# Kernel tuning notes

Measured on AMD Instinct MI355X. Metric: run time of the kernel, lower is better.

Reference implementation:

```python
import jax, jax.numpy as jnp
import numpy as np

N_HEAD = 16
QK_NOPE = 128
QK_ROPE = 64
QK_HEAD = QK_NOPE + QK_ROPE  # 192
V_HEAD = 128
SCALE = 1.0 / np.sqrt(QK_HEAD)


def setup_inputs() -> dict:
    key = jax.random.key(0)
    ks = jax.random.split(key, 8)
    B, T, C = 2, 2048, 2048
    s = lambda fan: 1.0 / np.sqrt(fan)
    return {
        "x": jax.random.normal(ks[0], (B, T, C), jnp.float32),
        "freqs_cis": jax.random.uniform(ks[1], (T, QK_ROPE // 2, 2), jnp.float32),
        "w_q": jax.random.normal(ks[2], (C, N_HEAD * QK_HEAD), jnp.float32) * s(C),
        "w_kv_down": jax.random.normal(ks[3], (C, 256), jnp.float32) * s(C),
        "w_k_up": jax.random.normal(ks[4], (256, N_HEAD * QK_HEAD), jnp.float32) * s(256),
        "w_v_up": jax.random.normal(ks[5], (256, N_HEAD * V_HEAD), jnp.float32) * s(256),
        "w_o": jax.random.normal(ks[6], (N_HEAD * V_HEAD, C), jnp.float32) * s(N_HEAD * V_HEAD),
        "start_pos": 0,
    }


def _rotate_half(x):
    x1, x2 = x[..., : x.shape[-1] // 2], x[..., x.shape[-1] // 2 :]
    return jnp.concatenate([-x2, x1], axis=-1)


def reference(x, freqs_cis, w_q, w_kv_down, w_k_up, w_v_up, w_o, start_pos):
    B, T, C = x.shape
    # low-rank MLA projections
    q = (x @ w_q).reshape(B, T, N_HEAD, QK_HEAD)
    kv = x @ w_kv_down                                  # (B,T,r)
    k = (kv @ w_k_up).reshape(B, T, N_HEAD, QK_HEAD)
    v = (kv @ w_v_up).reshape(B, T, N_HEAD, V_HEAD)

    # inline RoPE on decoupled rope dims
    q_nope, q_rope = q[..., :QK_NOPE], q[..., QK_NOPE:]
    k_nope, k_rope = k[..., :QK_NOPE], k[..., QK_NOPE:]
    freqs = freqs_cis[start_pos : start_pos + T]         # (T, 32, 2)
    cos = freqs[..., 0][None, :, None, :]                # (1,T,1,32)
    sin = freqs[..., 1][None, :, None, :]
    rep = QK_ROPE // cos.shape[-1]
    cos = jnp.tile(cos, (1, 1, 1, rep))                  # (1,T,1,64)
    sin = jnp.tile(sin, (1, 1, 1, rep))
    q_rope = q_rope * cos + _rotate_half(q_rope) * sin
    k_rope = k_rope * cos + _rotate_half(k_rope) * sin
    q = jnp.concatenate([q_nope, q_rope], axis=-1)
    k = jnp.concatenate([k_nope, k_rope], axis=-1)

    # causal SDPA with mismatched QK vs V head dims
    scores = jnp.einsum("bqhd,bkhd->bhqk", q, k) * SCALE
    causal = jnp.tril(jnp.ones((T, T), dtype=bool))
    scores = jnp.where(causal[None, None], scores, -jnp.inf)
    probs = jax.nn.softmax(scores, axis=-1)
    out = jnp.einsum("bhqk,bkhd->bqhd", probs, v)        # (B,T,H,V_HEAD)
    out = out.reshape(B, T, N_HEAD * V_HEAD)
    return out @ w_o
```

## Files before the change

kernel.cpp:

```cpp
#include <hip/hip_runtime.h>
#include <stdint.h>

typedef unsigned short u16;
typedef float f32x4 __attribute__((ext_vector_type(4)));
typedef __bf16 bf16x8 __attribute__((ext_vector_type(8)));

static __device__ __forceinline__ u16 f2bf(float f) {
  union { float f; unsigned u; } v; v.f = f;
  unsigned r = v.u + 0x7fffu + ((v.u >> 16) & 1u);
  return (u16)(r >> 16);
}
static __device__ __forceinline__ float bf2f(u16 h) {
  union { unsigned u; float f; } v; v.u = ((unsigned)h) << 16;
  return v.f;
}

#define GLD_LDS16(gp, lp) __builtin_amdgcn_global_load_lds( \
    (__attribute__((address_space(1))) void*)(gp),          \
    (__attribute__((address_space(3))) void*)(lp), 16, 0, 0)

#define MFMA16(a, b, c) __builtin_amdgcn_mfma_f32_16x16x32_bf16((a), (b), (c), 0, 0, 0)

__global__ void prep_kernel(const float* __restrict__ x, u16* __restrict__ xb,
                            const float* __restrict__ w_q, u16* __restrict__ wqT,
                            const float* __restrict__ w_kvd, u16* __restrict__ wkdT,
                            const float* __restrict__ w_ku, u16* __restrict__ wkuT,
                            const float* __restrict__ w_vu, u16* __restrict__ wvuT,
                            const float* __restrict__ w_o, u16* __restrict__ woT) {
  __shared__ float tile[32][33];
  const int bid = blockIdx.x;
  const int tx = threadIdx.x, ty = threadIdx.y;
  if (bid < 2048) {
    const int tid = ty * 32 + tx;
    const long n = 4096ll * 2048;
    const long stride = 2048ll * 256 * 4;
    for (long i = ((long)bid * 256 + tid) * 4; i < n; i += stride) {
      float4 v = *(const float4*)(x + i);
      union { u16 s[4]; uint2 u; } pk;
      pk.s[0] = f2bf(v.x); pk.s[1] = f2bf(v.y); pk.s[2] = f2bf(v.z); pk.s[3] = f2bf(v.w);
      *(uint2*)(xb + i) = pk.u;
    }
    return;
  }
  const float* W; u16* WT; int K, N, bx, by;
  int r = bid - 2048;
  if (r < 6144)        { W = w_q;   WT = wqT;  K = 2048; N = 3072; bx = r % 96; by = r / 96; }
  else if ((r -= 6144) < 512) { W = w_kvd; WT = wkdT; K = 2048; N = 256;  bx = r % 8;  by = r / 8; }
  else if ((r -= 512) < 768)  { W = w_ku;  WT = wkuT; K = 256;  N = 3072; bx = r % 96; by = r / 96; }
  else if ((r -= 768) < 512)  { W = w_vu;  WT = wvuT; K = 256;  N = 2048; bx = r % 64; by = r / 64; }
  else                 { r -= 512; W = w_o; WT = woT; K = 2048; N = 2048; bx = r % 64; by = r / 64; }
  const int n0 = bx * 32, k0 = by * 32;
#pragma unroll
  for (int i = 0; i < 32; i += 8) tile[ty + i][tx] = W[(long)(k0 + ty + i) * N + n0 + tx];
  __syncthreads();
#pragma unroll
  for (int i = 0; i < 32; i += 8)
    WT[(long)(n0 + ty + i) * K + k0 + tx] = f2bf(tile[tx][ty + i]);
}

__device__ __forceinline__ void epilogue_rope_store(
    u16* __restrict__ C, const int N, const f32x4 (*acc)[4],
    const int m0, const int wr, const int wc, const int cbase_wave,
    const int lrow, const int lg, const bool ropewin,
    const float* __restrict__ freqs, const int sp) {
#pragma unroll
  for (int mi = 0; mi < 4; mi++) {
    const int r0 = m0 + (wr << 6) + (mi << 4) + (lg << 2);
#pragma unroll
    for (int r = 0; r < 4; r++) {
      float v0 = acc[mi][0][r], v1 = acc[mi][1][r];
      float v2 = acc[mi][2][r], v3 = acc[mi][3][r];
      if (ropewin) {
        const int t = (r0 + r) & 2047;
        const float2 cs0 = *(const float2*)&freqs[((long)(sp + t) * 32 + lrow) * 2];
        const float2 cs1 = *(const float2*)&freqs[((long)(sp + t) * 32 + 16 + lrow) * 2];
        const float n0v = v0 * cs0.x - v2 * cs0.y;
        const float n1v = v1 * cs1.x - v3 * cs1.y;
        const float n2v = v2 * cs0.x + v0 * cs0.y;
        const float n3v = v3 * cs1.x + v1 * cs1.y;
        v0 = n0v; v1 = n1v; v2 = n2v; v3 = n3v;
      }
      const long ro = (long)(r0 + r) * N + cbase_wave + lrow;
      C[ro] = f2bf(v0);
      C[ro + 16] = f2bf(v1);
      C[ro + 32] = f2bf(v2);
      C[ro + 48] = f2bf(v3);
    }
  }
}

__global__ __launch_bounds__(256, 2)
void gemm_q_kvd_kernel(const u16* __restrict__ A, const u16* __restrict__ wqT,
                       const u16* __restrict__ wkdT, u16* __restrict__ qb,
                       u16* __restrict__ kvb,
                       const float* __restrict__ freqs, const int* __restrict__ sp_ptr) {
  constexpr int K = 2048;
  const int bid = blockIdx.x;
  const int xcd = bid & 7;
  const int idx = bid >> 3;
  const int m0 = ((xcd << 2) + (idx & 3)) << 7;
  const int n0raw = (idx >> 2) << 7;
  const bool is_kv = n0raw >= 3072;
  const u16* BT = is_kv ? (wkdT + (long)(n0raw - 3072) * K) : (wqT + (long)n0raw * K);
  u16* C = is_kv ? kvb : qb;
  const int N = is_kv ? 256 : 3072;
  const int c_base = is_kv ? (n0raw - 3072) : n0raw;
  __shared__ alignas(16) u16 lA[128 * 64];
  __shared__ alignas(16) u16 lB[128 * 64];
  const int tid = threadIdx.x;
  const int w = tid >> 6, l = tid & 63;
  const int wr = w >> 1, wc = w & 1;
  const int lrow = l & 15, lg = l >> 4;
  const int srow = l >> 3, scol = (l & 7) << 3;
  f32x4 acc[4][4] = {};
  for (int kt = 0; kt < K; kt += 64) {
    __syncthreads();
#pragma unroll
    for (int i = 0; i < 4; i++) {
      const int chunk = (w << 2) + i;
      const int row = (chunk << 3) + srow;
      GLD_LDS16(A + (long)(m0 + row) * K + kt + scol, &lA[chunk << 9]);
      GLD_LDS16(BT + (long)row * K + kt + scol, &lB[chunk << 9]);
    }
    __syncthreads();
#pragma unroll
    for (int kk = 0; kk < 2; kk++) {
      bf16x8 af[4], bb[4];
#pragma unroll
      for (int i = 0; i < 4; i++) {
        af[i] = *(const bf16x8*)&lA[((wr << 6) + (i << 4) + lrow) * 64 + (kk << 5) + (lg << 3)];
        bb[i] = *(const bf16x8*)&lB[((wc << 6) + (i << 4) + lrow) * 64 + (kk << 5) + (lg << 3)];
      }
#pragma unroll
      for (int mi = 0; mi < 4; mi++)
#pragma unroll
        for (int ni = 0; ni < 4; ni++)
          acc[mi][ni] = MFMA16(af[mi], bb[ni], acc[mi][ni]);
    }
  }
  const int cbase_wave = c_base + (wc << 6);
  const bool ropewin = (!is_kv) && (cbase_wave % 192 == 128);
  const int sp = sp_ptr[0];
  epilogue_rope_store(C, N, acc, m0, wr, wc, cbase_wave, lrow, lg, ropewin, freqs, sp);
}

__global__ __launch_bounds__(256, 2)
void gemm_kup_vt_kernel(const u16* __restrict__ kvb, const u16* __restrict__ wkuT,
                        const u16* __restrict__ wvuT, u16* __restrict__ kb,
                        u16* __restrict__ vTb,
                        const float* __restrict__ freqs, const int* __restrict__ sp_ptr) {
  constexpr int K = 256;
  const int bid = blockIdx.x;
  const u16 *A, *BT;
  u16* C;
  int N, m0, n0;
  bool is_k;
  if (bid < 768) {
    const int xcd = bid & 7, idx = bid >> 3;
    A = kvb; BT = wkuT; C = kb; N = 3072;
    m0 = ((xcd << 2) + (idx & 3)) << 7;
    n0 = (idx >> 2) << 7;
    is_k = true;
  } else {
    const int r = bid - 768;
    const int xcd = r & 7, idx = r >> 3;
    const int mt = (xcd << 1) + (idx & 1);
    const int rest = idx >> 1;
    const int nt = rest & 15, bz = rest >> 4;
    A = wvuT; BT = kvb + (long)bz * 2048 * 256; C = vTb + (long)bz * 2048 * 2048;
    N = 2048;
    m0 = mt << 7; n0 = nt << 7;
    is_k = false;
  }
  __shared__ alignas(16) u16 lA[128 * 64];
  __shared__ alignas(16) u16 lB[128 * 64];
  const int tid = threadIdx.x;
  const int w = tid >> 6, l = tid & 63;
  const int wr = w >> 1, wc = w & 1;
  const int lrow = l & 15, lg = l >> 4;
  const int srow = l >> 3, scol = (l & 7) << 3;
  f32x4 acc[4][4] = {};
  for (int kt = 0; kt < K; kt += 64) {
    __syncthreads();
#pragma unroll
    for (int i = 0; i < 4; i++) {
      const int chunk = (w << 2) + i;
      const int row = (chunk << 3) + srow;
      GLD_LDS16(A + (long)(m0 + row) * K + kt + scol, &lA[chunk << 9]);
      GLD_LDS16(BT + (long)(n0 + row) * K + kt + scol, &lB[chunk << 9]);
    }
    __syncthreads();
#pragma unroll
    for (int kk = 0; kk < 2; kk++) {
      bf16x8 af[4], bb[4];
#pragma unroll
      for (int i = 0; i < 4; i++) {
        af[i] = *(const bf16x8*)&lA[((wr << 6) + (i << 4) + lrow) * 64 + (kk << 5) + (lg << 3)];
        bb[i] = *(const bf16x8*)&lB[((wc << 6) + (i << 4) + lrow) * 64 + (kk << 5) + (lg << 3)];
      }
#pragma unroll
      for (int mi = 0; mi < 4; mi++)
#pragma unroll
        for (int ni = 0; ni < 4; ni++)
          acc[mi][ni] = MFMA16(af[mi], bb[ni], acc[mi][ni]);
    }
  }
  const int cbase_wave = n0 + (wc << 6);
  const bool ropewin = is_k && (cbase_wave % 192 == 128);
  const int sp = sp_ptr[0];
  epilogue_rope_store(C, N, acc, m0, wr, wc, cbase_wave, lrow, lg, ropewin, freqs, sp);
}

__global__ __launch_bounds__(256, 2)
void gemm_out_kernel(const u16* __restrict__ A, const u16* __restrict__ BT,
                     float* __restrict__ C) {
  constexpr int K = 2048, N = 2048;
  const int bid = blockIdx.x;
  const int xcd = bid & 7, idx = bid >> 3;
  const int m0 = ((xcd << 2) + (idx & 3)) << 7;
  const int n0 = (idx >> 2) << 7;
  __shared__ alignas(16) u16 lA[128 * 64];
  __shared__ alignas(16) u16 lB[128 * 64];
  const int tid = threadIdx.x;
  const int w = tid >> 6, l = tid & 63;
  const int wr = w >> 1, wc = w & 1;
  const int lrow = l & 15, lg = l >> 4;
  const int srow = l >> 3, scol = (l & 7) << 3;
  f32x4 acc[4][4] = {};
  for (int kt = 0; kt < K; kt += 64) {
    __syncthreads();
#pragma unroll
    for (int i = 0; i < 4; i++) {
      const int chunk = (w << 2) + i;
      const int row = (chunk << 3) + srow;
      GLD_LDS16(A + (long)(m0 + row) * K + kt + scol, &lA[chunk << 9]);
      GLD_LDS16(BT + (long)(n0 + row) * K + kt + scol, &lB[chunk << 9]);
    }
    __syncthreads();
#pragma unroll
    for (int kk = 0; kk < 2; kk++) {
      bf16x8 af[4], bb[4];
#pragma unroll
      for (int i = 0; i < 4; i++) {
        af[i] = *(const bf16x8*)&lA[((wr << 6) + (i << 4) + lrow) * 64 + (kk << 5) + (lg << 3)];
        bb[i] = *(const bf16x8*)&lB[((wc << 6) + (i << 4) + lrow) * 64 + (kk << 5) + (lg << 3)];
      }
#pragma unroll
      for (int mi = 0; mi < 4; mi++)
#pragma unroll
        for (int ni = 0; ni < 4; ni++)
          acc[mi][ni] = MFMA16(af[mi], bb[ni], acc[mi][ni]);
    }
  }
#pragma unroll
  for (int mi = 0; mi < 4; mi++) {
    const int r0 = m0 + (wr << 6) + (mi << 4) + (lg << 2);
#pragma unroll
    for (int ni = 0; ni < 4; ni++) {
      const int c0 = n0 + (wc << 6) + (ni << 4) + lrow;
#pragma unroll
      for (int r = 0; r < 4; r++)
        C[(long)(r0 + r) * N + c0] = acc[mi][ni][r];
    }
  }
}


__device__ __forceinline__ void attn_tile_step(
    const bf16x8* __restrict__ qf, f32x4* __restrict__ o, float* __restrict__ l_part,
    const int qrb, const int t0,
    const u16* __restrict__ Kl, const u16* __restrict__ Vl,
    u16* __restrict__ pw, const int lrow, const int lg) {
  constexpr float SCALE = 0.07216878364870323f;
  f32x4 s[4];
  __builtin_amdgcn_s_setprio(1);
#pragma unroll
  for (int tb = 0; tb < 4; tb++) {
    f32x4 a = {};
#pragma unroll
    for (int kb = 0; kb < 6; kb++) {
      bf16x8 kf = *(const bf16x8*)&Kl[((tb << 4) + lrow) * 200 + (kb << 5) + (lg << 3)];
      a = MFMA16(qf[kb], kf, a);
    }
    s[tb] = a;
  }
  __builtin_amdgcn_s_setprio(0);
#pragma unroll
  for (int tb = 0; tb < 4; tb++) {
    const int tt = t0 + (tb << 4) + lrow;
#pragma unroll
    for (int r = 0; r < 4; r++) {
      const int qrow = qrb + (lg << 2) + r;
      float p = __expf(s[tb][r] * SCALE);
      p = (tt <= qrow) ? p : 0.f;
      s[tb][r] = p;
      l_part[r] += p;
    }
  }
#pragma unroll
  for (int tb = 0; tb < 4; tb++)
#pragma unroll
    for (int r = 0; r < 4; r++)
      pw[((lg << 2) + r) * 68 + (tb << 4) + lrow] = f2bf(s[tb][r]);
  bf16x8 pf0 = *(const bf16x8*)&pw[lrow * 68 + (lg << 3)];
  bf16x8 pf1 = *(const bf16x8*)&pw[lrow * 68 + 32 + (lg << 3)];
  __builtin_amdgcn_s_setprio(1);
#pragma unroll
  for (int db = 0; db < 8; db++) {
    bf16x8 v0 = *(const bf16x8*)&Vl[((db << 4) + lrow) * 72 + (lg << 3)];
    bf16x8 v1 = *(const bf16x8*)&Vl[((db << 4) + lrow) * 72 + 32 + (lg << 3)];
    o[db] = MFMA16(pf0, v0, o[db]);
    o[db] = MFMA16(pf1, v1, o[db]);
  }
  __builtin_amdgcn_s_setprio(0);
}

__device__ __forceinline__ void attn_tile_step2(
    const bf16x8* __restrict__ qfA, const bf16x8* __restrict__ qfB,
    f32x4* __restrict__ oA, f32x4* __restrict__ oB,
    float* __restrict__ lpA, float* __restrict__ lpB,
    const int qrbA, const int qrbB, const int t0,
    const u16* __restrict__ Kl, const u16* __restrict__ Vl,
    u16* __restrict__ pwA, u16* __restrict__ pwB, const int lrow, const int lg) {
  constexpr float SCALE = 0.07216878364870323f;
  f32x4 sA[4], sB[4];
  __builtin_amdgcn_s_setprio(1);
#pragma unroll
  for (int tb = 0; tb < 4; tb++) {
    f32x4 a = {}, bq = {};
#pragma unroll
    for (int kb = 0; kb < 6; kb++) {
      bf16x8 kf = *(const bf16x8*)&Kl[((tb << 4) + lrow) * 200 + (kb << 5) + (lg << 3)];
      a = MFMA16(qfA[kb], kf, a);
      bq = MFMA16(qfB[kb], kf, bq);
    }
    sA[tb] = a;
    sB[tb] = bq;
  }
  __builtin_amdgcn_s_setprio(0);
#pragma unroll
  for (int tb = 0; tb < 4; tb++) {
    const int tt = t0 + (tb << 4) + lrow;
#pragma unroll
    for (int r = 0; r < 4; r++) {
      const int qrowA = qrbA + (lg << 2) + r;
      float pA = __expf(sA[tb][r] * SCALE);
      pA = (tt <= qrowA) ? pA : 0.f;
      sA[tb][r] = pA;
      lpA[r] += pA;
      const int qrowB = qrbB + (lg << 2) + r;
      float pB = __expf(sB[tb][r] * SCALE);
      pB = (tt <= qrowB) ? pB : 0.f;
      sB[tb][r] = pB;
      lpB[r] += pB;
    }
  }
#pragma unroll
  for (int tb = 0; tb < 4; tb++)
#pragma unroll
    for (int r = 0; r < 4; r++) {
      pwA[((lg << 2) + r) * 68 + (tb << 4) + lrow] = f2bf(sA[tb][r]);
      pwB[((lg << 2) + r) * 68 + (tb << 4) + lrow] = f2bf(sB[tb][r]);
    }
  bf16x8 pfA0 = *(const bf16x8*)&pwA[lrow * 68 + (lg << 3)];
  bf16x8 pfA1 = *(const bf16x8*)&pwA[lrow * 68 + 32 + (lg << 3)];
  bf16x8 pfB0 = *(const bf16x8*)&pwB[lrow * 68 + (lg << 3)];
  bf16x8 pfB1 = *(const bf16x8*)&pwB[lrow * 68 + 32 + (lg << 3)];
  __builtin_amdgcn_s_setprio(1);
#pragma unroll
  for (int db = 0; db < 8; db++) {
    bf16x8 v0 = *(const bf16x8*)&Vl[((db << 4) + lrow) * 72 + (lg << 3)];
    bf16x8 v1 = *(const bf16x8*)&Vl[((db << 4) + lrow) * 72 + 32 + (lg << 3)];
    oA[db] = MFMA16(pfA0, v0, oA[db]);
    oB[db] = MFMA16(pfB0, v0, oB[db]);
    oA[db] = MFMA16(pfA1, v1, oA[db]);
    oB[db] = MFMA16(pfB1, v1, oB[db]);
  }
  __builtin_amdgcn_s_setprio(0);
}

__device__ __forceinline__ void attn_write(
    u16* __restrict__ ob, const f32x4* __restrict__ o, const float* __restrict__ l_part,
    const int lrow, const int lg) {
#pragma unroll
  for (int r = 0; r < 4; r++) {
    float l = l_part[r];
#pragma unroll
    for (int d = 1; d < 16; d <<= 1) l += __shfl_xor(l, d);
    const float inv = 1.f / l;
#pragma unroll
    for (int db = 0; db < 8; db++)
      ob[(long)((lg << 2) + r) * 2048 + (db << 4) + lrow] = f2bf(o[db][r] * inv);
  }
}

__global__ __launch_bounds__(256, 2)
void attn_kernel(const u16* __restrict__ q, const u16* __restrict__ k,
                 const u16* __restrict__ vT, u16* __restrict__ out) {
  const int bid = blockIdx.x;
  const int xcd = bid & 7;
  const int rest = bid >> 3;
  const int pair = rest & 15;
  const int bh = ((rest >> 4) << 3) | xcd;
  const int b = bh >> 4, h = bh & 15;
  const int tid = threadIdx.x, w = tid >> 6, l = tid & 63;
  const int lrow = l & 15, lg = l >> 4;
  const int qtA = pair, qtB = 31 - pair;
  const int qrbA = (qtA << 6) + (w << 4);
  const int qrbB = (qtB << 6) + (w << 4);
  __shared__ alignas(16) u16 Kl[64 * 200];
  __shared__ alignas(16) u16 Vl[128 * 72];
  __shared__ alignas(16) u16 Pl[4][2][16 * 68];

  bf16x8 qfA[6], qfB[6];
  {
    const u16* qbA = q + ((long)b * 2048 + qrbA + lrow) * 3072 + h * 192;
    const u16* qbB = q + ((long)b * 2048 + qrbB + lrow) * 3072 + h * 192;
#pragma unroll
    for (int kb = 0; kb < 6; kb++) {
      qfA[kb] = *(const bf16x8*)&qbA[(kb << 5) + (lg << 3)];
      qfB[kb] = *(const bf16x8*)&qbB[(kb << 5) + (lg << 3)];
    }
  }
  f32x4 oA[8] = {}, oB[8] = {};
  float lA[4] = {}, lB[4] = {};

  const u16* kbh = k + (long)b * 2048 * 3072 + h * 192;
  const u16* vbh = vT + ((long)b * 2048 + h * 128) * 2048;
  const int tEndA = qtA << 6, tEndB = qtB << 6;

  for (int t0 = 0; t0 <= tEndB; t0 += 64) {
    __syncthreads();
#pragma unroll
    for (int i = 0; i < 6; i++) {
      int c = (i << 8) + tid;
      int row = c / 24, col = (c % 24) << 3;
      *(bf16x8*)&Kl[row * 200 + col] = *(const bf16x8*)&kbh[(long)(t0 + row) * 3072 + col];
    }
#pragma unroll
    for (int i = 0; i < 4; i++) {
      int c = (i << 8) + tid;
      int row = c >> 3, col = (c & 7) << 3;
      *(bf16x8*)&Vl[row * 72 + col] = *(const bf16x8*)&vbh[(long)row * 2048 + t0 + col];
    }
    __syncthreads();
    if (t0 <= tEndA)
      attn_tile_step2(qfA, qfB, oA, oB, lA, lB, qrbA, qrbB, t0, Kl, Vl,
                      &Pl[w][0][0], &Pl[w][1][0], lrow, lg);
    else
      attn_tile_step(qfB, oB, lB, qrbB, t0, Kl, Vl, &Pl[w][1][0], lrow, lg);
  }
  attn_write(out + ((long)b * 2048 + qrbA) * 2048 + (h << 7), oA, lA, lrow, lg);
  attn_write(out + ((long)b * 2048 + qrbB) * 2048 + (h << 7), oB, lB, lrow, lg);
}

extern "C" void kernel_launch(void* const* d_in, const int* in_sizes, int n_in,
                              void* d_out, int out_size, void* d_ws, size_t ws_size,
                              hipStream_t stream) {
  const float* x = (const float*)d_in[0];
  const float* fcis = (const float*)d_in[1];
  const float* w_q = (const float*)d_in[2];
  const float* w_kvd = (const float*)d_in[3];
  const float* w_ku = (const float*)d_in[4];
  const float* w_vu = (const float*)d_in[5];
  const float* w_o = (const float*)d_in[6];
  const int* start_pos = (const int*)d_in[7];
  float* out = (float*)d_out;

  char* p = (char*)d_ws;
  auto alloc = [&](long bytes) -> char* {
    char* r = p;
    p += (bytes + 255) & ~255ll;
    return r;
  };
  u16* xb = (u16*)alloc(4096ll * 2048 * 2);
  u16* wqT = (u16*)alloc(3072ll * 2048 * 2);
  u16* wkdT = (u16*)alloc(256ll * 2048 * 2);
  u16* wkuT = (u16*)alloc(3072ll * 256 * 2);
  u16* wvuT = (u16*)alloc(2048ll * 256 * 2);
  u16* woT = (u16*)alloc(2048ll * 2048 * 2);
  u16* qb = (u16*)alloc(4096ll * 3072 * 2);
  u16* kvb = (u16*)alloc(4096ll * 256 * 2);
  u16* kb = (u16*)alloc(4096ll * 3072 * 2);
  u16* aob = (u16*)alloc(4096ll * 2048 * 2);
  u16* vTb = xb;

  prep_kernel<<<14080, dim3(32, 8), 0, stream>>>(x, xb, w_q, wqT, w_kvd, wkdT,
                                                 w_ku, wkuT, w_vu, wvuT, w_o, woT);
  gemm_q_kvd_kernel<<<832, 256, 0, stream>>>(xb, wqT, wkdT, qb, kvb, fcis, start_pos);
  gemm_kup_vt_kernel<<<1280, 256, 0, stream>>>(kvb, wkuT, wvuT, kb, vTb, fcis, start_pos);
  attn_kernel<<<512, 256, 0, stream>>>(qb, kb, vTb, aob);
  gemm_out_kernel<<<512, 256, 0, stream>>>(aob, woT, out);
}
```

Baseline: 274.1 us.

## Split attention KV range across two blocks and merge partials in a norm kernel

Each query-tile pair's key range is split into two halves handled by separate blocks, doubling the attention grid. Each block writes unnormalized bf16 partial outputs and row sums, and a new kernel adds the partials and normalizes. The aim is finer-grained parallelism and shorter per-block work in the attention stage. In exchange it adds extra global traffic and a kernel launch, and it stores unnormalized partials in bf16, which could cost accuracy. The merge assumes both halves share the same exponent reference, so correctness depends on how the softmax max is handled.

```diff
diff --git a/kernel.cpp b/kernel.cpp
--- a/kernel.cpp
+++ b/kernel.cpp
@@ -379,35 +379,41 @@
   __builtin_amdgcn_s_setprio(0);
 }
 
-__device__ __forceinline__ void attn_write(
-    u16* __restrict__ ob, const f32x4* __restrict__ o, const float* __restrict__ l_part,
+__device__ __forceinline__ void attn_write_part(
+    u16* __restrict__ op, float* __restrict__ lp,
+    const f32x4* __restrict__ o, const float* __restrict__ l_part,
     const int lrow, const int lg) {
 #pragma unroll
   for (int r = 0; r < 4; r++) {
     float l = l_part[r];
 #pragma unroll
     for (int d = 1; d < 16; d <<= 1) l += __shfl_xor(l, d);
-    const float inv = 1.f / l;
+    if (lrow == 0) lp[(long)((lg << 2) + r) * 16] = l;
 #pragma unroll
     for (int db = 0; db < 8; db++)
-      ob[(long)((lg << 2) + r) * 2048 + (db << 4) + lrow] = f2bf(o[db][r] * inv);
+      op[(long)((lg << 2) + r) * 2048 + (db << 4) + lrow] = f2bf(o[db][r]);
   }
 }
 
 __global__ __launch_bounds__(256, 2)
 void attn_kernel(const u16* __restrict__ q, const u16* __restrict__ k,
-                 const u16* __restrict__ vT, u16* __restrict__ out) {
+                 const u16* __restrict__ vT,
+                 u16* __restrict__ o0p, u16* __restrict__ o1p,
+                 float* __restrict__ l0p, float* __restrict__ l1p) {
   const int bid = blockIdx.x;
   const int xcd = bid & 7;
   const int rest = bid >> 3;
   const int pair = rest & 15;
-  const int bh = ((rest >> 4) << 3) | xcd;
+  const int s = (rest >> 4) & 1;
+  const int bh = ((rest >> 5) << 3) | xcd;
   const int b = bh >> 4, h = bh & 15;
   const int tid = threadIdx.x, w = tid >> 6, l = tid & 63;
   const int lrow = l & 15, lg = l >> 4;
   const int qtA = pair, qtB = 31 - pair;
   const int qrbA = (qtA << 6) + (w << 4);
   const int qrbB = (qtB << 6) + (w << 4);
+  const int EA = qtA + 1, EB = qtB + 1;
+  const int hA = (EA + 1) >> 1, hB = (EB + 1) >> 1;
   __shared__ alignas(16) u16 Kl[64 * 200];
   __shared__ alignas(16) u16 Vl[128 * 72];
   __shared__ alignas(16) u16 Pl[4][2][16 * 68];
@@ -427,9 +433,8 @@
 
   const u16* kbh = k + (long)b * 2048 * 3072 + h * 192;
   const u16* vbh = vT + ((long)b * 2048 + h * 128) * 2048;
-  const int tEndA = qtA << 6, tEndB = qtB << 6;
-
-  for (int t0 = 0; t0 <= tEndB; t0 += 64) {
+
+  auto stage = [&](int t0) {
     __syncthreads();
 #pragma unroll
     for (int i = 0; i < 6; i++) {
@@ -444,14 +449,52 @@
       *(bf16x8*)&Vl[row * 72 + col] = *(const bf16x8*)&vbh[(long)row * 2048 + t0 + col];
     }
     __syncthreads();
-    if (t0 <= tEndA)
-      attn_tile_step2(qfA, qfB, oA, oB, lA, lB, qrbA, qrbB, t0, Kl, Vl,
-                      &Pl[w][0][0], &Pl[w][1][0], lrow, lg);
-    else
+  };
+
+  if (s == 0) {
+    for (int T = 0; T < hB; T++) {
+      const int t0 = T << 6;
+      stage(t0);
+      if (T < hA)
+        attn_tile_step2(qfA, qfB, oA, oB, lA, lB, qrbA, qrbB, t0, Kl, Vl,
+                        &Pl[w][0][0], &Pl[w][1][0], lrow, lg);
+      else
+        attn_tile_step(qfB, oB, lB, qrbB, t0, Kl, Vl, &Pl[w][1][0], lrow, lg);
+    }
+  } else {
+    for (int T = hA; T < EA; T++) {
+      const int t0 = T << 6;
+      stage(t0);
+      attn_tile_step(qfA, oA, lA, qrbA, t0, Kl, Vl, &Pl[w][0][0], lrow, lg);
+    }
+    for (int T = hB; T < EB; T++) {
+      const int t0 = T << 6;
+      stage(t0);
       attn_tile_step(qfB, oB, lB, qrbB, t0, Kl, Vl, &Pl[w][1][0], lrow, lg);
-  }
-  attn_write(out + ((long)b * 2048 + qrbA) * 2048 + (h << 7), oA, lA, lrow, lg);
-  attn_write(out + ((long)b * 2048 + qrbB) * 2048 + (h << 7), oB, lB, lrow, lg);
+    }
+  }
+  u16* op = s ? o1p : o0p;
+  float* lp = s ? l1p : l0p;
+  attn_write_part(op + ((long)b * 2048 + qrbA) * 2048 + (h << 7),
+                  lp + ((long)b * 2048 + qrbA) * 16 + h, oA, lA, lrow, lg);
+  attn_write_part(op + ((long)b * 2048 + qrbB) * 2048 + (h << 7),
+                  lp + ((long)b * 2048 + qrbB) * 16 + h, oB, lB, lrow, lg);
+}
+
+__global__ void attn_norm_kernel(const u16* __restrict__ o0, const u16* __restrict__ o1,
+                                 const float* __restrict__ l0, const float* __restrict__ l1,
+                                 u16* __restrict__ aob) {
+  const long i8 = ((long)blockIdx.x * 256 + threadIdx.x) << 3;
+  const int row = (int)(i8 >> 11);
+  const int h = ((int)i8 & 2047) >> 7;
+  const float linv = 1.f / (l0[row * 16 + h] + l1[row * 16 + h]);
+  union { u16 s[8]; uint4 u; } pa, pb, po;
+  pa.u = *(const uint4*)(o0 + i8);
+  pb.u = *(const uint4*)(o1 + i8);
+#pragma unroll
+  for (int j = 0; j < 8; j++)
+    po.s[j] = f2bf((bf2f(pa.s[j]) + bf2f(pb.s[j])) * linv);
+  *(uint4*)(aob + i8) = po.u;
 }
 
 extern "C" void kernel_launch(void* const* d_in, const int* in_sizes, int n_in,
@@ -474,21 +517,31 @@
     return r;
   };
   u16* xb = (u16*)alloc(4096ll * 2048 * 2);
+  u16* qb = (u16*)alloc(4096ll * 3072 * 2);
+  u16* kb = (u16*)alloc(4096ll * 3072 * 2);
+  u16* aob = (u16*)alloc(4096ll * 2048 * 2);
+  u16* woT = (u16*)alloc(2048ll * 2048 * 2);
+  char* pool = p;
   u16* wqT = (u16*)alloc(3072ll * 2048 * 2);
   u16* wkdT = (u16*)alloc(256ll * 2048 * 2);
   u16* wkuT = (u16*)alloc(3072ll * 256 * 2);
   u16* wvuT = (u16*)alloc(2048ll * 256 * 2);
-  u16* woT = (u16*)alloc(2048ll * 2048 * 2);
-  u16* qb = (u16*)alloc(4096ll * 3072 * 2);
   u16* kvb = (u16*)alloc(4096ll * 256 * 2);
-  u16* kb = (u16*)alloc(4096ll * 3072 * 2);
-  u16* aob = (u16*)alloc(4096ll * 2048 * 2);
+  u16* o0p = (u16*)pool;
+  u16* o1p = (u16*)(pool + 16777216);
+  float* l0p = (float*)(pool + 2 * 16777216);
+  float* l1p = (float*)(pool + 2 * 16777216 + 262144);
+  {
+    char* endp = pool + 2 * 16777216 + 2 * 262144;
+    if (endp > p) p = endp;
+  }
   u16* vTb = xb;
 
   prep_kernel<<<14080, dim3(32, 8), 0, stream>>>(x, xb, w_q, wqT, w_kvd, wkdT,
                                                  w_ku, wkuT, w_vu, wvuT, w_o, woT);
   gemm_q_kvd_kernel<<<832, 256, 0, stream>>>(xb, wqT, wkdT, qb, kvb, fcis, start_pos);
   gemm_kup_vt_kernel<<<1280, 256, 0, stream>>>(kvb, wkuT, wvuT, kb, vTb, fcis, start_pos);
-  attn_kernel<<<512, 256, 0, stream>>>(qb, kb, vTb, aob);
+  attn_kernel<<<1024, 256, 0, stream>>>(qb, kb, vTb, o0p, o1p, l0p, l1p);
+  attn_norm_kernel<<<4096, 256, 0, stream>>>(o0p, o1p, l0p, l1p, aob);
   gemm_out_kernel<<<512, 256, 0, stream>>>(aob, woT, out);
 }
```

Result: no change. 278.3 us (+1.5%).

## Load attention K/V tiles via direct global-to-LDS loads with XOR swizzle

Applied to the files above, without the earlier changes.

The attention kernel now stages its K and V tiles with global_load_lds 16-byte direct copies instead of going through registers. The LDS layout drops the row padding and uses an XOR swizzle on the 16-byte chunk index, with global source addresses permuted to match, so MFMA fragment reads stay free of bank conflicts. This removes the VGPR round-trip and the padding, and shrinks LDS use. It relies on wave-contiguous LDS destination ordering matching the swizzled global addressing, and there is still no double buffering.

```diff
diff --git a/kernel.cpp b/kernel.cpp
--- a/kernel.cpp
+++ b/kernel.cpp
@@ -266,12 +266,17 @@
 }
 
 
+__device__ __forceinline__ const u16* kaddr(const u16* Kl, int tb, int lrow, int jr_sw) {
+  return &Kl[((tb << 4) + lrow) * 192 + (jr_sw << 3)];
+}
+
 __device__ __forceinline__ void attn_tile_step(
     const bf16x8* __restrict__ qf, f32x4* __restrict__ o, float* __restrict__ l_part,
     const int qrb, const int t0,
     const u16* __restrict__ Kl, const u16* __restrict__ Vl,
     u16* __restrict__ pw, const int lrow, const int lg) {
   constexpr float SCALE = 0.07216878364870323f;
+  const int ks = lrow & 7;
   f32x4 s[4];
   __builtin_amdgcn_s_setprio(1);
 #pragma unroll
@@ -279,7 +284,9 @@
     f32x4 a = {};
 #pragma unroll
     for (int kb = 0; kb < 6; kb++) {
-      bf16x8 kf = *(const bf16x8*)&Kl[((tb << 4) + lrow) * 200 + (kb << 5) + (lg << 3)];
+      const int jr = (kb << 2) + lg;
+      const int jr_sw = (jr & 24) | ((jr & 7) ^ ks);
+      bf16x8 kf = *(const bf16x8*)kaddr(Kl, tb, lrow, jr_sw);
       a = MFMA16(qf[kb], kf, a);
     }
     s[tb] = a;
@@ -304,11 +311,13 @@
       pw[((lg << 2) + r) * 68 + (tb << 4) + lrow] = f2bf(s[tb][r]);
   bf16x8 pf0 = *(const bf16x8*)&pw[lrow * 68 + (lg << 3)];
   bf16x8 pf1 = *(const bf16x8*)&pw[lrow * 68 + 32 + (lg << 3)];
+  const int vc0 = (lg ^ ks) << 3, vc1 = ((4 + lg) ^ ks) << 3;
   __builtin_amdgcn_s_setprio(1);
 #pragma unroll
   for (int db = 0; db < 8; db++) {
-    bf16x8 v0 = *(const bf16x8*)&Vl[((db << 4) + lrow) * 72 + (lg << 3)];
-    bf16x8 v1 = *(const bf16x8*)&Vl[((db << 4) + lrow) * 72 + 32 + (lg << 3)];
+    const int vrow = ((db << 4) + lrow) << 6;
+    bf16x8 v0 = *(const bf16x8*)&Vl[vrow + vc0];
+    bf16x8 v1 = *(const bf16x8*)&Vl[vrow + vc1];
     o[db] = MFMA16(pf0, v0, o[db]);
     o[db] = MFMA16(pf1, v1, o[db]);
   }
@@ -323,6 +332,7 @@
     const u16* __restrict__ Kl, const u16* __restrict__ Vl,
     u16* __restrict__ pwA, u16* __restrict__ pwB, const int lrow, const int lg) {
   constexpr float SCALE = 0.07216878364870323f;
+  const int ks = lrow & 7;
   f32x4 sA[4], sB[4];
   __builtin_amdgcn_s_setprio(1);
 #pragma unroll
@@ -330,7 +340,9 @@
     f32x4 a = {}, bq = {};
 #pragma unroll
     for (int kb = 0; kb < 6; kb++) {
-      bf16x8 kf = *(const bf16x8*)&Kl[((tb << 4) + lrow) * 200 + (kb << 5) + (lg << 3)];
+      const int jr = (kb << 2) + lg;
+      const int jr_sw = (jr & 24) | ((jr & 7) ^ ks);
+      bf16x8 kf = *(const bf16x8*)kaddr(Kl, tb, lrow, jr_sw);
       a = MFMA16(qfA[kb], kf, a);
       bq = MFMA16(qfB[kb], kf, bq);
     }
@@ -366,11 +378,13 @@
   bf16x8 pfA1 = *(const bf16x8*)&pwA[lrow * 68 + 32 + (lg << 3)];
   bf16x8 pfB0 = *(const bf16x8*)&pwB[lrow * 68 + (lg << 3)];
   bf16x8 pfB1 = *(const bf16x8*)&pwB[lrow * 68 + 32 + (lg << 3)];
+  const int vc0 = (lg ^ ks) << 3, vc1 = ((4 + lg) ^ ks) << 3;
   __builtin_amdgcn_s_setprio(1);
 #pragma unroll
   for (int db = 0; db < 8; db++) {
-    bf16x8 v0 = *(const bf16x8*)&Vl[((db << 4) + lrow) * 72 + (lg << 3)];
-    bf16x8 v1 = *(const bf16x8*)&Vl[((db << 4) + lrow) * 72 + 32 + (lg << 3)];
+    const int vrow = ((db << 4) + lrow) << 6;
+    bf16x8 v0 = *(const bf16x8*)&Vl[vrow + vc0];
+    bf16x8 v1 = *(const bf16x8*)&Vl[vrow + vc1];
     oA[db] = MFMA16(pfA0, v0, oA[db]);
     oB[db] = MFMA16(pfB0, v0, oB[db]);
     oA[db] = MFMA16(pfA1, v1, oA[db]);
@@ -408,8 +422,8 @@
   const int qtA = pair, qtB = 31 - pair;
   const int qrbA = (qtA << 6) + (w << 4);
   const int qrbB = (qtB << 6) + (w << 4);
-  __shared__ alignas(16) u16 Kl[64 * 200];
-  __shared__ alignas(16) u16 Vl[128 * 72];
+  __shared__ alignas(16) u16 Kl[64 * 192];
+  __shared__ alignas(16) u16 Vl[128 * 64];
   __shared__ alignas(16) u16 Pl[4][2][16 * 68];
 
   bf16x8 qfA[6], qfB[6];
@@ -429,20 +443,30 @@
   const u16* vbh = vT + ((long)b * 2048 + h * 128) * 2048;
   const int tEndA = qtA << 6, tEndB = qtB << 6;
 
+  int krow_[6], kcol_[6], vrow_[4], vcol_[4];
+#pragma unroll
+  for (int i = 0; i < 6; i++) {
+    const int c = (i << 8) + tid;
+    krow_[i] = c / 24;
+    const int j = c % 24;
+    kcol_[i] = ((j & 24) | ((j & 7) ^ (krow_[i] & 7))) << 3;
+  }
+#pragma unroll
+  for (int i = 0; i < 4; i++) {
+    const int c = (i << 8) + tid;
+    vrow_[i] = c >> 3;
+    vcol_[i] = ((c & 7) ^ (vrow_[i] & 7)) << 3;
+  }
+  const int wbase = (tid & ~63) << 3;
+
   for (int t0 = 0; t0 <= tEndB; t0 += 64) {
     __syncthreads();
 #pragma unroll
-    for (int i = 0; i < 6; i++) {
-      int c = (i << 8) + tid;
-      int row = c / 24, col = (c % 24) << 3;
-      *(bf16x8*)&Kl[row * 200 + col] = *(const bf16x8*)&kbh[(long)(t0 + row) * 3072 + col];
-    }
-#pragma unroll
-    for (int i = 0; i < 4; i++) {
-      int c = (i << 8) + tid;
-      int row = c >> 3, col = (c & 7) << 3;
-      *(bf16x8*)&Vl[row * 72 + col] = *(const bf16x8*)&vbh[(long)row * 2048 + t0 + col];
-    }
+    for (int i = 0; i < 6; i++)
+      GLD_LDS16(kbh + (long)(t0 + krow_[i]) * 3072 + kcol_[i], &Kl[(i << 11) + wbase]);
+#pragma unroll
+    for (int i = 0; i < 4; i++)
+      GLD_LDS16(vbh + (long)vrow_[i] * 2048 + t0 + vcol_[i], &Vl[(i << 11) + wbase]);
     __syncthreads();
     if (t0 <= tEndA)
       attn_tile_step2(qfA, qfB, oA, oB, lA, lB, qrbA, qrbB, t0, Kl, Vl,
```

After: 263.9 us. -3.7%, faster.
